# Performance work log

Measured on AMD Instinct MI355X. Metric: run time of the kernel, lower is better.

The kernel has to match this reference:

```python
import jax, jax.numpy as jnp
import numpy as np
import math

D_MODEL = 1024
N_HEADS = 16
HEAD_DIM = D_MODEL // N_HEADS
BATCH = 2
SEQ = 2048


def setup_inputs() -> dict:
    key = jax.random.key(0)
    ks = jax.random.split(key, 6)
    x = jax.random.normal(ks[0], (BATCH, SEQ, D_MODEL), dtype=jnp.float32)
    # causal additive mask, finite large negative
    causal = jnp.tril(jnp.ones((SEQ, SEQ), dtype=bool))
    attn_mask = jnp.where(causal, 0.0, -1e9).astype(jnp.float32)[None, None, :, :]
    s = 1.0 / math.sqrt(D_MODEL)
    W_qkv = jax.random.uniform(ks[1], (3 * D_MODEL, D_MODEL), jnp.float32, -s, s)
    b_qkv = jax.random.uniform(ks[2], (3 * D_MODEL,), jnp.float32, -s, s)
    W_out = jax.random.uniform(ks[3], (D_MODEL, D_MODEL), jnp.float32, -s, s)
    b_out = jax.random.uniform(ks[4], (D_MODEL,), jnp.float32, -s, s)
    return {"x": x, "attn_mask": attn_mask, "W_qkv": W_qkv, "b_qkv": b_qkv,
            "W_out": W_out, "b_out": b_out}


def reference(x, attn_mask, W_qkv, b_qkv, W_out, b_out):
    batch, seq, _ = x.shape
    # torch Linear: x @ W^T + b
    qkv = x @ W_qkv.T + b_qkv                              # [B,S,3D]
    qkv = qkv.reshape(batch, seq, 3, N_HEADS, HEAD_DIM)
    qkv = jnp.transpose(qkv, (2, 0, 3, 1, 4))              # [3,B,H,S,hd]
    q, k, v = qkv[0], qkv[1], qkv[2]
    scores = jnp.einsum('bhsd,bhtd->bhst', q, k) / math.sqrt(HEAD_DIM)
    scores = scores + attn_mask
    attn = jax.nn.softmax(scores, axis=-1)                 # dropout p=0 (eval)
    context = jnp.einsum('bhst,bhtd->bhsd', attn, v)       # [B,H,S,hd]
    context = jnp.transpose(context, (0, 2, 1, 3)).reshape(batch, seq, D_MODEL)
    return context @ W_out.T + b_out
```

## Files before the change

### kernel.cpp

```cpp
#include <hip/hip_runtime.h>
#include <hip/hip_bf16.h>

#define BATCH 2
#define SEQ 2048
#define DMODEL 1024
#define NHEADS 16
#define HDIM 64
#define MROWS (BATCH*SEQ)

typedef short bf16x8_t __attribute__((ext_vector_type(8)));
typedef float f32x4_t __attribute__((ext_vector_type(4)));

union Frag { uint4 u; bf16x8_t b; };

__device__ __forceinline__ unsigned short f2bf(float f) {
  union { __hip_bfloat16 h; unsigned short s; } u;
  u.h = __float2bfloat16(f);
  return u.s;
}

__device__ __forceinline__ void gload16(const unsigned short* g, unsigned short* l) {
  __builtin_amdgcn_global_load_lds(
      (const __attribute__((address_space(1))) unsigned int*)(const void*)g,
      (__attribute__((address_space(3))) unsigned int*)(void*)l,
      16, 0, 0);
}

__global__ void cvt3_kernel(const float* __restrict__ a, const float* __restrict__ b,
                            const float* __restrict__ c,
                            unsigned short* __restrict__ oa, unsigned short* __restrict__ ob,
                            unsigned short* __restrict__ oc,
                            int na, int nb, int nc) {
  const int n = na + nb + nc;
  for (int i = blockIdx.x * blockDim.x + threadIdx.x; i < n;
       i += gridDim.x * blockDim.x) {
    const float* src; unsigned short* dst; int j;
    if (i < na)           { src = a; dst = oa; j = i; }
    else if (i < na + nb) { src = b; dst = ob; j = i - na; }
    else                  { src = c; dst = oc; j = i - na - nb; }
    float4 v = reinterpret_cast<const float4*>(src)[j];
    ushort4 o;
    o.x = f2bf(v.x); o.y = f2bf(v.y); o.z = f2bf(v.z); o.w = f2bf(v.w);
    reinterpret_cast<ushort4*>(dst)[j] = o;
  }
}

#define QSCALE 0.18033688011112042f


__launch_bounds__(256)
__global__ void qkv_gemm_kernel(const unsigned short* __restrict__ A,
                                const unsigned short* __restrict__ Bw,
                                const float* __restrict__ bias,
                                unsigned short* __restrict__ qb,
                                unsigned short* __restrict__ kb,
                                unsigned short* __restrict__ vb) {
  __shared__ __align__(16) unsigned short As[2 * 128 * 32];
  __shared__ __align__(16) unsigned short Bs[2 * 128 * 32];
  const int tid = threadIdx.x;
  const int w = tid >> 6, lane = tid & 63;
  const int rr = lane & 15, cg = lane >> 4;
  const int wr = w >> 1, wc = w & 1;
  const int kswz = (rr >> 1) & 3;
  const int bm = blockIdx.x * 128, bn = blockIdx.y * 128;

  const int cid0 = (w * 2) * 64 + lane, cid1 = (w * 2 + 1) * 64 + lane;
  const int rowA0 = cid0 >> 2, kc0 = (cid0 & 3) ^ ((cid0 >> 3) & 3);
  const int rowA1 = cid1 >> 2, kc1 = (cid1 & 3) ^ ((cid1 >> 3) & 3);
  const unsigned short* gA0 = A + (size_t)(bm + rowA0) * DMODEL + kc0 * 8;
  const unsigned short* gA1 = A + (size_t)(bm + rowA1) * DMODEL + kc1 * 8;
  const unsigned short* gB0 = Bw + (size_t)(bn + rowA0) * DMODEL + kc0 * 8;
  const unsigned short* gB1 = Bw + (size_t)(bn + rowA1) * DMODEL + kc1 * 8;
  unsigned short* lA0 = As + (w * 2) * 512;
  unsigned short* lA1 = As + (w * 2 + 1) * 512;
  unsigned short* lB0 = Bs + (w * 2) * 512;
  unsigned short* lB1 = Bs + (w * 2 + 1) * 512;

#define GSTAGE(bi_, k0_) do {                       \
    gload16(gA0 + (k0_), lA0 + (bi_) * 4096);       \
    gload16(gA1 + (k0_), lA1 + (bi_) * 4096);       \
    gload16(gB0 + (k0_), lB0 + (bi_) * 4096);       \
    gload16(gB1 + (k0_), lB1 + (bi_) * 4096);       \
  } while (0)

  f32x4_t acc[4][4];
#pragma unroll
  for (int i = 0; i < 4; ++i)
#pragma unroll
    for (int j = 0; j < 4; ++j) acc[i][j] = (f32x4_t){0.f, 0.f, 0.f, 0.f};

  GSTAGE(0, 0);
  for (int it = 0; it < DMODEL / 32; ++it) {
    __syncthreads();
    if (it + 1 < DMODEL / 32) GSTAGE((it + 1) & 1, (it + 1) * 32);
    const uint4* A4 = reinterpret_cast<const uint4*>(As) + (it & 1) * 512;
    const uint4* B4 = reinterpret_cast<const uint4*>(Bs) + (it & 1) * 512;
    Frag af[4], bf[4];
#pragma unroll
    for (int mt = 0; mt < 4; ++mt)
      af[mt].u = A4[(wr * 64 + 16 * mt + rr) * 4 + (cg ^ kswz)];
#pragma unroll
    for (int nt = 0; nt < 4; ++nt)
      bf[nt].u = B4[(wc * 64 + 16 * nt + rr) * 4 + (cg ^ kswz)];
    __builtin_amdgcn_s_setprio(1);
#pragma unroll
    for (int mt = 0; mt < 4; ++mt)
#pragma unroll
      for (int nt = 0; nt < 4; ++nt)
        acc[mt][nt] = __builtin_amdgcn_mfma_f32_16x16x32_bf16(af[mt].b, bf[nt].b, acc[mt][nt], 0, 0, 0);
    __builtin_amdgcn_s_setprio(0);
  }
#undef GSTAGE

#pragma unroll
  for (int nt = 0; nt < 4; ++nt) {
    const int m = bn + wc * 64 + 16 * nt + rr;
    const float bv = bias[m];
    const int which = m >> 10;
    const int h = (m & 1023) >> 6;
    const int d = m & 63;
#pragma unroll
    for (int mt = 0; mt < 4; ++mt) {
#pragma unroll
      for (int r = 0; r < 4; ++r) {
        const int n = bm + wr * 64 + 16 * mt + cg * 4 + r;
        const int b = n >> 11, sq = n & (SEQ - 1);
        const int bh = b * NHEADS + h;
        float val = acc[mt][nt][r] + bv;
        if (which == 0) {
          qb[((size_t)bh * SEQ + sq) * HDIM + d] = f2bf(val * QSCALE);
        } else if (which == 1) {
          kb[((size_t)bh * SEQ + sq) * HDIM + d] = f2bf(val);
        } else {
          vb[((size_t)bh * HDIM + d) * SEQ + sq] = f2bf(val);
        }
      }
    }
  }
}

__launch_bounds__(256)
__global__ void out_gemm_kernel(const unsigned short* __restrict__ A,
                                const unsigned short* __restrict__ Bw,
                                const float* __restrict__ bias,
                                float* __restrict__ out) {
  __shared__ __align__(16) unsigned short As[2 * 128 * 32];
  __shared__ __align__(16) unsigned short Bs[2 * 128 * 32];
  const int tid = threadIdx.x;
  const int w = tid >> 6, lane = tid & 63;
  const int rr = lane & 15, cg = lane >> 4;
  const int wr = w >> 1, wc = w & 1;
  const int kswz = (rr >> 1) & 3;
  const int bm = blockIdx.x * 128, bn = blockIdx.y * 128;

  const int cid0 = (w * 2) * 64 + lane, cid1 = (w * 2 + 1) * 64 + lane;
  const int rowA0 = cid0 >> 2, kc0 = (cid0 & 3) ^ ((cid0 >> 3) & 3);
  const int rowA1 = cid1 >> 2, kc1 = (cid1 & 3) ^ ((cid1 >> 3) & 3);
  const unsigned short* gA0 = A + (size_t)(bm + rowA0) * DMODEL + kc0 * 8;
  const unsigned short* gA1 = A + (size_t)(bm + rowA1) * DMODEL + kc1 * 8;
  const unsigned short* gB0 = Bw + (size_t)(bn + rowA0) * DMODEL + kc0 * 8;
  const unsigned short* gB1 = Bw + (size_t)(bn + rowA1) * DMODEL + kc1 * 8;
  unsigned short* lA0 = As + (w * 2) * 512;
  unsigned short* lA1 = As + (w * 2 + 1) * 512;
  unsigned short* lB0 = Bs + (w * 2) * 512;
  unsigned short* lB1 = Bs + (w * 2 + 1) * 512;

#define GSTAGE(bi_, k0_) do {                       \
    gload16(gA0 + (k0_), lA0 + (bi_) * 4096);       \
    gload16(gA1 + (k0_), lA1 + (bi_) * 4096);       \
    gload16(gB0 + (k0_), lB0 + (bi_) * 4096);       \
    gload16(gB1 + (k0_), lB1 + (bi_) * 4096);       \
  } while (0)

  f32x4_t acc[4][4];
#pragma unroll
  for (int i = 0; i < 4; ++i)
#pragma unroll
    for (int j = 0; j < 4; ++j) acc[i][j] = (f32x4_t){0.f, 0.f, 0.f, 0.f};

  GSTAGE(0, 0);
  for (int it = 0; it < DMODEL / 32; ++it) {
    __syncthreads();
    if (it + 1 < DMODEL / 32) GSTAGE((it + 1) & 1, (it + 1) * 32);
    const uint4* A4 = reinterpret_cast<const uint4*>(As) + (it & 1) * 512;
    const uint4* B4 = reinterpret_cast<const uint4*>(Bs) + (it & 1) * 512;
    Frag af[4], bf[4];
#pragma unroll
    for (int mt = 0; mt < 4; ++mt)
      af[mt].u = A4[(wr * 64 + 16 * mt + rr) * 4 + (cg ^ kswz)];
#pragma unroll
    for (int nt = 0; nt < 4; ++nt)
      bf[nt].u = B4[(wc * 64 + 16 * nt + rr) * 4 + (cg ^ kswz)];
    __builtin_amdgcn_s_setprio(1);
#pragma unroll
    for (int mt = 0; mt < 4; ++mt)
#pragma unroll
      for (int nt = 0; nt < 4; ++nt)
        acc[mt][nt] = __builtin_amdgcn_mfma_f32_16x16x32_bf16(af[mt].b, bf[nt].b, acc[mt][nt], 0, 0, 0);
    __builtin_amdgcn_s_setprio(0);
  }
#undef GSTAGE

#pragma unroll
  for (int nt = 0; nt < 4; ++nt) {
    const int m = bn + wc * 64 + 16 * nt + rr;
    const float bv = bias[m];
#pragma unroll
    for (int mt = 0; mt < 4; ++mt) {
#pragma unroll
      for (int r = 0; r < 4; ++r) {
        const int n = bm + wr * 64 + 16 * mt + cg * 4 + r;
        out[(size_t)n * DMODEL + m] = acc[mt][nt][r] + bv;
      }
    }
  }
}

__launch_bounds__(256, 4)
__global__ void attn_kernel(const unsigned short* __restrict__ qb,
                            const unsigned short* __restrict__ kb,
                            const unsigned short* __restrict__ vb,
                            unsigned short* __restrict__ ctx) {
  __shared__ __align__(16) uint4 Ks[2][512];
  __shared__ __align__(16) uint4 Vs[2][512];

  const int tid = threadIdx.x;
  const int w = tid >> 6, lane = tid & 63;
  const int rr = lane & 15, cg = lane >> 4;
  const int rxw = rr & 7;
  const int bh = blockIdx.x;
  const int c = 31 - blockIdx.y;

  const unsigned short* Kbh = kb + (size_t)bh * SEQ * HDIM;
  const unsigned short* Vbh = vb + (size_t)bh * HDIM * SEQ;

  const int j0 = w * 2, j1 = w * 2 + 1;
  const int cid0 = j0 * 64 + lane, cid1 = j1 * 64 + lane;
  const int row0 = cid0 >> 3, ch0 = cid0 & 7;
  const int row1 = cid1 >> 3, ch1 = cid1 & 7;
  const int kOff0 = row0 * HDIM + ((ch0 ^ (row0 & 7)) << 3);
  const int kOff1 = row1 * HDIM + ((ch1 ^ (row1 & 7)) << 3);
  const int vOff0 = row0 * SEQ + ((ch0 ^ (row0 & 7)) << 3);
  const int vOff1 = row1 * SEQ + ((ch1 ^ (row1 & 7)) << 3);

#define STAGE(bi, tb_) do {                                             \
    const unsigned short* Kt_ = Kbh + (size_t)(tb_) * HDIM;             \
    const unsigned short* Vt_ = Vbh + (tb_);                            \
    unsigned short* kl_ = (unsigned short*)&Ks[bi][0];                  \
    unsigned short* vl_ = (unsigned short*)&Vs[bi][0];                  \
    gload16(Kt_ + kOff0, kl_ + j0 * 512);                               \
    gload16(Kt_ + kOff1, kl_ + j1 * 512);                               \
    gload16(Vt_ + vOff0, vl_ + j0 * 512);                               \
    gload16(Vt_ + vOff1, vl_ + j1 * 512);                               \
  } while (0)

  const int b = bh >> 4, h = bh & 15;
  const int s_base = c * 64 + w * 16;
  const int nt = c + 1;

  STAGE(0, 0);

  Frag q0, q1;
  {
    const unsigned short* qrow = qb + ((size_t)bh * SEQ + (s_base + rr)) * HDIM;
    q0.u = *reinterpret_cast<const uint4*>(qrow + cg * 8);
    q1.u = *reinterpret_cast<const uint4*>(qrow + 32 + cg * 8);
  }

  f32x4_t acc[4];
#pragma unroll
  for (int i = 0; i < 4; ++i) acc[i] = (f32x4_t){0.f, 0.f, 0.f, 0.f};
  float mreg = -1e30f;
  float lp = 0.f;

  for (int t = 0; t < nt; ++t) {
    __syncthreads();
    if (t + 1 < nt) STAGE((t + 1) & 1, (t + 1) * 64);
    const uint4* Kt = &Ks[t & 1][0];
    const uint4* Vt = &Vs[t & 1][0];

    f32x4_t s[4];
    __builtin_amdgcn_s_setprio(1);
#pragma unroll
    for (int st = 0; st < 4; ++st) {
      s[st] = (f32x4_t){0.f, 0.f, 0.f, 0.f};
      Frag kf;
      kf.u = Kt[(st * 16 + rr) * 8 + (cg ^ rxw)];
      s[st] = __builtin_amdgcn_mfma_f32_16x16x32_bf16(kf.b, q0.b, s[st], 0, 0, 0);
      kf.u = Kt[(st * 16 + rr) * 8 + ((4 + cg) ^ rxw)];
      s[st] = __builtin_amdgcn_mfma_f32_16x16x32_bf16(kf.b, q1.b, s[st], 0, 0, 0);
    }
    __builtin_amdgcn_s_setprio(0);

    if (t == nt - 1) {
#pragma unroll
      for (int st = 0; st < 4; ++st)
#pragma unroll
        for (int r = 0; r < 4; ++r)
          if (st * 16 + cg * 4 + r > w * 16 + rr) s[st][r] = -1e30f;
    }

    float mx = s[0][0];
#pragma unroll
    for (int st = 0; st < 4; ++st)
#pragma unroll
      for (int r = 0; r < 4; ++r) mx = fmaxf(mx, s[st][r]);
    if (__any(mx > mreg + 11.0f)) {
      float m = fmaxf(mx, __shfl_xor(mx, 16));
      m = fmaxf(m, __shfl_xor(m, 32));
      m = fmaxf(m, mreg);
      const float alpha = exp2f(mreg - m);
      mreg = m;
      lp *= alpha;
      float av[4];
#pragma unroll
      for (int r = 0; r < 4; ++r) av[r] = __shfl(alpha, cg * 4 + r);
#pragma unroll
      for (int dt = 0; dt < 4; ++dt)
#pragma unroll
        for (int r = 0; r < 4; ++r) acc[dt][r] *= av[r];
    }

    float pv[4][4];
#pragma unroll
    for (int st = 0; st < 4; ++st)
#pragma unroll
      for (int r = 0; r < 4; ++r) {
        pv[st][r] = exp2f(s[st][r] - mreg);
        lp += pv[st][r];
      }

    unsigned int uu[4][2];
#pragma unroll
    for (int st = 0; st < 4; ++st)
#pragma unroll
      for (int i = 0; i < 2; ++i)
        asm("v_cvt_pk_bf16_f32 %0, %1, %2"
            : "=v"(uu[st][i]) : "v"(pv[st][2 * i]), "v"(pv[st][2 * i + 1]));

    Frag pA0, pA1;
#pragma unroll
    for (int s2 = 0; s2 < 2; ++s2) {
#pragma unroll
      for (int i = 0; i < 2; ++i) {
        unsigned int x = uu[2 * s2][i], y = uu[2 * s2 + 1][i];
        asm("v_permlane32_swap_b32 %0, %1" : "+v"(x), "+v"(y));
        asm("v_permlane16_swap_b32 %0, %1" : "+v"(x), "+v"(y));
        if (s2 == 0) { pA0.u[i] = x; pA0.u[2 + i] = y; }
        else         { pA1.u[i] = x; pA1.u[2 + i] = y; }
      }
    }

    __builtin_amdgcn_s_setprio(1);
#pragma unroll
    for (int dt = 0; dt < 4; ++dt) {
      Frag vf;
      vf.u = Vt[(dt * 16 + rr) * 8 + (cg ^ rxw)];
      acc[dt] = __builtin_amdgcn_mfma_f32_16x16x32_bf16(pA0.b, vf.b, acc[dt], 0, 0, 0);
      vf.u = Vt[(dt * 16 + rr) * 8 + ((4 + cg) ^ rxw)];
      acc[dt] = __builtin_amdgcn_mfma_f32_16x16x32_bf16(pA1.b, vf.b, acc[dt], 0, 0, 0);
    }
    __builtin_amdgcn_s_setprio(0);
  }

  float ls = lp + __shfl_xor(lp, 16);
  ls += __shfl_xor(ls, 32);
  const float inv = 1.0f / ls;
  float iv[4];
#pragma unroll
  for (int r = 0; r < 4; ++r) iv[r] = __shfl(inv, cg * 4 + r);
#pragma unroll
  for (int r = 0; r < 4; ++r) {
    const int sq = s_base + cg * 4 + r;
    unsigned short* crow = ctx + (size_t)(b * SEQ + sq) * DMODEL + h * HDIM;
#pragma unroll
    for (int dt = 0; dt < 4; ++dt)
      crow[dt * 16 + rr] = f2bf(acc[dt][r] * iv[r]);
  }
#undef STAGE
}

extern "C" void kernel_launch(void* const* d_in, const int* in_sizes, int n_in,
                              void* d_out, int out_size, void* d_ws, size_t ws_size,
                              hipStream_t stream) {
  const float* x    = (const float*)d_in[0];
  const float* Wqkv = (const float*)d_in[2];
  const float* bqkv = (const float*)d_in[3];
  const float* Wout = (const float*)d_in[4];
  const float* bout = (const float*)d_in[5];
  float* out = (float*)d_out;

  unsigned short* ws    = (unsigned short*)d_ws;
  unsigned short* xb    = ws;
  unsigned short* wqkvb = xb + (size_t)MROWS * DMODEL;
  unsigned short* woutb = wqkvb + (size_t)3 * DMODEL * DMODEL;
  unsigned short* qbuf  = woutb + (size_t)DMODEL * DMODEL;
  unsigned short* kbuf  = qbuf + (size_t)BATCH * NHEADS * SEQ * HDIM;
  unsigned short* vbuf  = kbuf + (size_t)BATCH * NHEADS * SEQ * HDIM;
  unsigned short* ctx   = vbuf + (size_t)BATCH * NHEADS * SEQ * HDIM;

  cvt3_kernel<<<2048, 256, 0, stream>>>(
      x, Wqkv, Wout, xb, wqkvb, woutb,
      MROWS * DMODEL / 4, 3 * DMODEL * DMODEL / 4, DMODEL * DMODEL / 4);

  qkv_gemm_kernel<<<dim3(MROWS / 128, 3 * DMODEL / 128), 256, 0, stream>>>(
      xb, wqkvb, bqkv, qbuf, kbuf, vbuf);

  attn_kernel<<<dim3(BATCH * NHEADS, SEQ / 64), 256, 0, stream>>>(
      qbuf, kbuf, vbuf, ctx);

  out_gemm_kernel<<<dim3(MROWS / 128, DMODEL / 128), 256, 0, stream>>>(
      ctx, woutb, bout, out);
}
```

Baseline: 115.2 us.

## Triple-buffer LDS in QKV and output GEMMs with two-stage-ahead prefetch

Both GEMM kernels move from a double-buffered LDS ring to a three-buffer ring. Global-to-LDS loads are issued two K-steps ahead, and a partial vmcnt wait is used in place of a full __syncthreads drain. The goal is to keep more global loads in flight so MFMA work is less often stalled on memory. In exchange, LDS use per block rises from 32KB to 48KB, which may lower occupancy, and correctness now relies on hand-written waitcnt counts.

```diff
diff --git a/kernel.cpp b/kernel.cpp
--- a/kernel.cpp
+++ b/kernel.cpp
@@ -55,8 +55,8 @@
                                 unsigned short* __restrict__ qb,
                                 unsigned short* __restrict__ kb,
                                 unsigned short* __restrict__ vb) {
-  __shared__ __align__(16) unsigned short As[2 * 128 * 32];
-  __shared__ __align__(16) unsigned short Bs[2 * 128 * 32];
+  __shared__ __align__(16) unsigned short As[3 * 4096];
+  __shared__ __align__(16) unsigned short Bs[3 * 4096];
   const int tid = threadIdx.x;
   const int w = tid >> 6, lane = tid & 63;
   const int rr = lane & 15, cg = lane >> 4;
@@ -90,11 +90,20 @@
     for (int j = 0; j < 4; ++j) acc[i][j] = (f32x4_t){0.f, 0.f, 0.f, 0.f};
 
   GSTAGE(0, 0);
-  for (int it = 0; it < DMODEL / 32; ++it) {
-    __syncthreads();
-    if (it + 1 < DMODEL / 32) GSTAGE((it + 1) & 1, (it + 1) * 32);
-    const uint4* A4 = reinterpret_cast<const uint4*>(As) + (it & 1) * 512;
-    const uint4* B4 = reinterpret_cast<const uint4*>(Bs) + (it & 1) * 512;
+  GSTAGE(1, 32);
+  int cur = 0;
+  for (int it = 0; it < 32; ++it) {
+    if (it < 31) asm volatile("s_waitcnt vmcnt(4)" ::: "memory");
+    else         asm volatile("s_waitcnt vmcnt(0)" ::: "memory");
+    __builtin_amdgcn_sched_barrier(0);
+    __builtin_amdgcn_s_barrier();
+    __builtin_amdgcn_sched_barrier(0);
+    if (it + 2 < 32) {
+      int nb2 = cur + 2; if (nb2 >= 3) nb2 -= 3;
+      GSTAGE(nb2, (it + 2) * 32);
+    }
+    const uint4* A4 = reinterpret_cast<const uint4*>(As) + cur * 512;
+    const uint4* B4 = reinterpret_cast<const uint4*>(Bs) + cur * 512;
     Frag af[4], bf[4];
 #pragma unroll
     for (int mt = 0; mt < 4; ++mt)
@@ -109,6 +118,7 @@
       for (int nt = 0; nt < 4; ++nt)
         acc[mt][nt] = __builtin_amdgcn_mfma_f32_16x16x32_bf16(af[mt].b, bf[nt].b, acc[mt][nt], 0, 0, 0);
     __builtin_amdgcn_s_setprio(0);
+    cur = (cur == 2) ? 0 : cur + 1;
   }
 #undef GSTAGE
 
@@ -144,8 +154,8 @@
                                 const unsigned short* __restrict__ Bw,
                                 const float* __restrict__ bias,
                                 float* __restrict__ out) {
-  __shared__ __align__(16) unsigned short As[2 * 128 * 32];
-  __shared__ __align__(16) unsigned short Bs[2 * 128 * 32];
+  __shared__ __align__(16) unsigned short As[3 * 4096];
+  __shared__ __align__(16) unsigned short Bs[3 * 4096];
   const int tid = threadIdx.x;
   const int w = tid >> 6, lane = tid & 63;
   const int rr = lane & 15, cg = lane >> 4;
@@ -179,11 +189,20 @@
     for (int j = 0; j < 4; ++j) acc[i][j] = (f32x4_t){0.f, 0.f, 0.f, 0.f};
 
   GSTAGE(0, 0);
-  for (int it = 0; it < DMODEL / 32; ++it) {
-    __syncthreads();
-    if (it + 1 < DMODEL / 32) GSTAGE((it + 1) & 1, (it + 1) * 32);
-    const uint4* A4 = reinterpret_cast<const uint4*>(As) + (it & 1) * 512;
-    const uint4* B4 = reinterpret_cast<const uint4*>(Bs) + (it & 1) * 512;
+  GSTAGE(1, 32);
+  int cur = 0;
+  for (int it = 0; it < 32; ++it) {
+    if (it < 31) asm volatile("s_waitcnt vmcnt(4)" ::: "memory");
+    else         asm volatile("s_waitcnt vmcnt(0)" ::: "memory");
+    __builtin_amdgcn_sched_barrier(0);
+    __builtin_amdgcn_s_barrier();
+    __builtin_amdgcn_sched_barrier(0);
+    if (it + 2 < 32) {
+      int nb2 = cur + 2; if (nb2 >= 3) nb2 -= 3;
+      GSTAGE(nb2, (it + 2) * 32);
+    }
+    const uint4* A4 = reinterpret_cast<const uint4*>(As) + cur * 512;
+    const uint4* B4 = reinterpret_cast<const uint4*>(Bs) + cur * 512;
     Frag af[4], bf[4];
 #pragma unroll
     for (int mt = 0; mt < 4; ++mt)
@@ -198,6 +217,7 @@
       for (int nt = 0; nt < 4; ++nt)
         acc[mt][nt] = __builtin_amdgcn_mfma_f32_16x16x32_bf16(af[mt].b, bf[nt].b, acc[mt][nt], 0, 0, 0);
     __builtin_amdgcn_s_setprio(0);
+    cur = (cur == 2) ? 0 : cur + 1;
   }
 #undef GSTAGE
 
```

After: 111.4 us. -3.3%, faster.
